# Performance work log

Hardware: AMD Instinct MI355X
Metric: run time of the kernel (lower is better)

Reference implementation:

```python
import jax, jax.numpy as jnp
import numpy as np

N_NODES = 100000
N_EDGES = 1600000
IN_DIM = 128
HID = 128
OUT_DIM = 64
N_LAYERS = 2
MAXK = 16


def setup_inputs() -> dict:
    key = jax.random.key(0)
    ks = jax.random.split(key, 8)
    x = jax.random.normal(ks[0], (N_NODES, IN_DIM), dtype=jnp.float32)
    src = jax.random.randint(ks[1], (N_EDGES,), 0, N_NODES, dtype=jnp.int32)
    dst = jax.random.randint(ks[2], (N_EDGES,), 0, N_NODES, dtype=jnp.int32)
    # Linear weights stored as [in, out] (y = x @ W + b), xavier-like scale
    s_in = float(np.sqrt(2.0 / (IN_DIM + HID)))
    s_h = float(np.sqrt(2.0 / (HID + HID)))
    s_out = float(np.sqrt(2.0 / (HID + OUT_DIM)))
    W_in = jax.random.normal(ks[3], (IN_DIM, HID), dtype=jnp.float32) * s_in
    b_in = jnp.zeros((HID,), dtype=jnp.float32)
    W_lin = jax.random.normal(ks[4], (N_LAYERS, HID, HID), dtype=jnp.float32) * s_h
    b_lin = jnp.zeros((N_LAYERS, HID), dtype=jnp.float32)
    eps = jnp.zeros((N_LAYERS,), dtype=jnp.float32)  # learn_eps=True, init_eps=0
    W_out = jax.random.normal(ks[5], (HID, OUT_DIM), dtype=jnp.float32) * s_out
    b_out = jnp.zeros((OUT_DIM,), dtype=jnp.float32)
    return {"x": x, "src": src, "dst": dst, "W_in": W_in, "b_in": b_in,
            "W_lin": W_lin, "b_lin": b_lin, "eps": eps,
            "W_out": W_out, "b_out": b_out}


def _maxk(x, k):
    # OPTMaxK: keep top-k entries per row (dim=1), zero the rest.
    _, idx = jax.lax.top_k(x, k)                      # [N, k]
    rows = jnp.arange(x.shape[0])[:, None]            # [N, 1]
    mask = jnp.zeros_like(x).at[rows, idx].set(1.0)
    return x * mask


def reference(x, src, dst, W_in, b_in, W_lin, b_lin, eps, W_out, b_out):
    n = x.shape[0]
    h = jax.nn.relu(x @ W_in + b_in)                  # lin_in + relu
    for i in range(N_LAYERS):
        h = h @ W_lin[i] + b_lin[i]                   # per-layer Linear
        h_sparse = _maxk(h, MAXK)                     # MaxK nonlinearity (dropout p=0 -> identity)
        # GIN sum aggregation over edges: neigh[v] = sum_{(u->v)} h_sparse[u]
        msg = jnp.take(h_sparse, src, axis=0)         # [E, HID] irregular gather
        neigh = jax.ops.segment_sum(msg, dst, num_segments=n)
        h = (1.0 + eps[i]) * h_sparse + neigh         # eps residual (apply_func=None, no norm)
    return h @ W_out + b_out
```

## Files before the change

kernel.cpp:

```cpp
#include <hip/hip_runtime.h>
#include <cstdint>
#include <cstddef>


typedef __attribute__((ext_vector_type(8))) short bf16x8;
typedef __attribute__((ext_vector_type(4))) float f32x4;

#define BSHIFT 8
#define NBUK 512

__device__ __forceinline__ unsigned rne_bf16(float v) {
  unsigned u = __float_as_uint(v);
  return (u + 0x7fffu + ((u >> 16) & 1u)) >> 16;
}

__global__ __launch_bounds__(256) void wt_build_all_kernel(
    const float* __restrict__ W_in, const float* __restrict__ W_lin,
    const float* __restrict__ W_out, short* __restrict__ out) {
  const int i = blockIdx.x * 256 + threadIdx.x;
  if (i >= 57344) return;
  const float* W;
  int nout, local;
  short* H;
  if (i < 16384) {
    W = W_in; nout = 128; local = i; H = out;
  } else if (i < 32768) {
    W = W_lin; nout = 128; local = i - 16384; H = out + 32768;
  } else if (i < 49152) {
    W = W_lin + 16384; nout = 128; local = i - 32768; H = out + 65536;
  } else {
    W = W_out; nout = 64; local = i - 49152; H = out + 98304;
  }
  const int nn = local >> 7, k = local & 127;
  const float v = W[k * nout + nn];
  const unsigned hb = rne_bf16(v);
  const float hf = __uint_as_float(hb << 16);
  const unsigned lb = rne_bf16(v - hf);
  H[local] = (short)hb;
  H[local + nout * 128] = (short)lb;
}

__global__ __launch_bounds__(256, 2) void gemm_in_kernel(
    const float* __restrict__ X, const short* __restrict__ WtH,
    const short* __restrict__ WtL, const float* __restrict__ bias,
    short* __restrict__ Yh, short* __restrict__ Yl, int nrows, int ntiles) {
  constexpr int NOUT = 128;
  constexpr int NT = NOUT / 16;
  constexpr int LDB = 128 * 2 + 16;
  constexpr int PLANE = NOUT * LDB;
  __shared__ char lds[2 * PLANE];

  const int tid = threadIdx.x;
  for (int u = tid; u < 2 * NOUT * 16; u += 256) {
    const int plane = u / (NOUT * 16);
    const int v = u % (NOUT * 16);
    const int nrow = v >> 4, seg = v & 15;
    const short* src = plane ? WtL : WtH;
    const float4 d = *(const float4*)&src[nrow * 128 + seg * 8];
    *(float4*)&lds[plane * PLANE + nrow * LDB + seg * 16] = d;
  }
  __syncthreads();

  const int lane = tid & 63;
  const int wv = tid >> 6;
  const int li = lane & 15;
  const int kg = lane >> 4;

  float bv[NT];
#pragma unroll
  for (int t = 0; t < NT; ++t) bv[t] = bias[t * 16 + li];

  for (int tile = blockIdx.x; tile < ntiles; tile += gridDim.x) {
    const int rowbase = tile * 256 + wv * 64;

    f32x4 acc[4][NT];
#pragma unroll
    for (int rg = 0; rg < 4; ++rg)
#pragma unroll
      for (int t = 0; t < NT; ++t) acc[rg][t] = (f32x4){0.f, 0.f, 0.f, 0.f};

#pragma unroll
    for (int c = 0; c < 4; ++c) {
      bf16x8 ah[4], al[4];
#pragma unroll
      for (int rg = 0; rg < 4; ++rg) {
        const int row = rowbase + rg * 16 + li;
        const int rowc = (row < nrows) ? row : (nrows - 1);
        const float* xrow = X + (size_t)rowc * 128 + c * 32 + kg * 8;
        const float4 p0 = *(const float4*)&xrow[0];
        const float4 p1 = *(const float4*)&xrow[4];
        const float f[8] = {p0.x, p0.y, p0.z, p0.w, p1.x, p1.y, p1.z, p1.w};
#pragma unroll
        for (int e = 0; e < 8; ++e) {
          const unsigned hb = rne_bf16(f[e]);
          const float hf = __uint_as_float(hb << 16);
          ah[rg][e] = (short)hb;
          al[rg][e] = (short)rne_bf16(f[e] - hf);
        }
      }
      const int kb = c * 64 + kg * 16;
#pragma unroll
      for (int t = 0; t < NT; ++t) {
        const int boff = (t * 16 + li) * LDB + kb;
        const bf16x8 bh = *(const bf16x8*)&lds[boff];
        const bf16x8 bl = *(const bf16x8*)&lds[PLANE + boff];
#pragma unroll
        for (int rg = 0; rg < 4; ++rg) {
          acc[rg][t] =
              __builtin_amdgcn_mfma_f32_16x16x32_bf16(al[rg], bh, acc[rg][t], 0, 0, 0);
          acc[rg][t] =
              __builtin_amdgcn_mfma_f32_16x16x32_bf16(ah[rg], bl, acc[rg][t], 0, 0, 0);
          acc[rg][t] =
              __builtin_amdgcn_mfma_f32_16x16x32_bf16(ah[rg], bh, acc[rg][t], 0, 0, 0);
        }
      }
    }

#pragma unroll
    for (int rg = 0; rg < 4; ++rg) {
      const int orow = rowbase + rg * 16 + kg * 4;
#pragma unroll
      for (int t = 0; t < NT; ++t) {
        const int col = t * 16 + li;
#pragma unroll
        for (int r = 0; r < 4; ++r) {
          const int rr = orow + r;
          if (rr < nrows) {
            const float o = fmaxf(acc[rg][t][r] + bv[t], 0.f);
            const unsigned hb = rne_bf16(o);
            const float hf = __uint_as_float(hb << 16);
            Yh[(size_t)rr * 128 + col] = (short)hb;
            Yl[(size_t)rr * 128 + col] = (short)rne_bf16(o - hf);
          }
        }
      }
    }
  }
}

template <int NOUT>
__global__ __launch_bounds__(256, 2) void gemm_pl_kernel(
    const short* __restrict__ Xh, const short* __restrict__ Xl,
    const short* __restrict__ WtH, const short* __restrict__ WtL,
    const float* __restrict__ bias, float* __restrict__ Y, int nrows,
    int ntiles) {
  constexpr int NT = NOUT / 16;
  constexpr int LDB = 128 * 2 + 16;
  constexpr int PLANE = NOUT * LDB;
  __shared__ char lds[2 * PLANE];

  const int tid = threadIdx.x;
  for (int u = tid; u < 2 * NOUT * 16; u += 256) {
    const int plane = u / (NOUT * 16);
    const int v = u % (NOUT * 16);
    const int nrow = v >> 4, seg = v & 15;
    const short* src = plane ? WtL : WtH;
    const float4 d = *(const float4*)&src[nrow * 128 + seg * 8];
    *(float4*)&lds[plane * PLANE + nrow * LDB + seg * 16] = d;
  }
  __syncthreads();

  const int lane = tid & 63;
  const int wv = tid >> 6;
  const int li = lane & 15;
  const int kg = lane >> 4;

  float bv[NT];
#pragma unroll
  for (int t = 0; t < NT; ++t) bv[t] = bias[t * 16 + li];

  for (int tile = blockIdx.x; tile < ntiles; tile += gridDim.x) {
    const int rowbase = tile * 256 + wv * 64;

    f32x4 acc[4][NT];
#pragma unroll
    for (int rg = 0; rg < 4; ++rg)
#pragma unroll
      for (int t = 0; t < NT; ++t) acc[rg][t] = (f32x4){0.f, 0.f, 0.f, 0.f};

#pragma unroll
    for (int c = 0; c < 4; ++c) {
      bf16x8 ah[4], al[4];
#pragma unroll
      for (int rg = 0; rg < 4; ++rg) {
        const int row = rowbase + rg * 16 + li;
        const int rowc = (row < nrows) ? row : (nrows - 1);
        ah[rg] = *(const bf16x8*)&Xh[(size_t)rowc * 128 + c * 32 + kg * 8];
        al[rg] = *(const bf16x8*)&Xl[(size_t)rowc * 128 + c * 32 + kg * 8];
      }
      const int kb = c * 64 + kg * 16;
#pragma unroll
      for (int t = 0; t < NT; ++t) {
        const int boff = (t * 16 + li) * LDB + kb;
        const bf16x8 bh = *(const bf16x8*)&lds[boff];
        const bf16x8 bl = *(const bf16x8*)&lds[PLANE + boff];
#pragma unroll
        for (int rg = 0; rg < 4; ++rg) {
          acc[rg][t] =
              __builtin_amdgcn_mfma_f32_16x16x32_bf16(al[rg], bh, acc[rg][t], 0, 0, 0);
          acc[rg][t] =
              __builtin_amdgcn_mfma_f32_16x16x32_bf16(ah[rg], bl, acc[rg][t], 0, 0, 0);
          acc[rg][t] =
              __builtin_amdgcn_mfma_f32_16x16x32_bf16(ah[rg], bh, acc[rg][t], 0, 0, 0);
        }
      }
    }

#pragma unroll
    for (int rg = 0; rg < 4; ++rg) {
      const int orow = rowbase + rg * 16 + kg * 4;
#pragma unroll
      for (int t = 0; t < NT; ++t) {
        const int col = t * 16 + li;
#pragma unroll
        for (int r = 0; r < 4; ++r) {
          const int rr = orow + r;
          if (rr < nrows) Y[(size_t)rr * NOUT + col] = acc[rg][t][r] + bv[t];
        }
      }
    }
  }
}

__global__ __launch_bounds__(256) void maxk_kernel(
    const float* __restrict__ T, unsigned char* __restrict__ Cs,
    float* __restrict__ Vs, int nrows) {
  const int lane = threadIdx.x & 63;
  const int wid = threadIdx.x >> 6;
  const int sub = lane >> 4;
  const int s = lane & 15;
  const int shift = sub * 16;
  const unsigned below = (1u << s) - 1u;
  const int nquads = (nrows + 3) / 4;

  for (int quad = blockIdx.x * 4 + wid; quad < nquads; quad += gridDim.x * 4) {
    const int row = quad * 4 + sub;
    const int rowc = (row < nrows) ? row : (nrows - 1);
    const float* Trow = T + (size_t)rowc * 128;

    float v[8];
    unsigned k[8];
#pragma unroll
    for (int j = 0; j < 8; ++j) {
      v[j] = Trow[j * 16 + s];
      const unsigned u = __float_as_uint(v[j]);
      k[j] = u ^ (((unsigned)((int)u >> 31)) | 0x80000000u);
    }

    unsigned P = 0;
    int kth = 16;
    int sz = 128;
    bool done = false;
    for (int b = 31; b >= 0; --b) {
      const unsigned tgt = (P >> b) | 1u;
      int c = 0;
#pragma unroll
      for (int j = 0; j < 8; ++j) {
        const unsigned long long bal = __ballot((k[j] >> b) == tgt);
        c += __popc((unsigned)((bal >> shift) & 0xFFFFull));
      }
      if (!done) {
        if (c >= kth) {
          P |= (1u << b);
          sz = c;
        } else {
          sz -= c;
          kth -= c;
        }
        done = (sz == kth);
      }
      if (__all(done)) break;
    }
    if (done) P -= 1u;

    unsigned gtm[8], eqm[8];
    int gt_total = 0;
#pragma unroll
    for (int j = 0; j < 8; ++j) {
      const unsigned long long gb = __ballot(k[j] > P);
      const unsigned long long eb = __ballot(k[j] == P);
      gtm[j] = (unsigned)((gb >> shift) & 0xFFFFull);
      eqm[j] = (unsigned)((eb >> shift) & 0xFFFFull);
      gt_total += __popc(gtm[j]);
    }
    const int need = 16 - gt_total;
    int gt_pre = 0, eq_pre = 0;
#pragma unroll
    for (int j = 0; j < 8; ++j) {
      const bool isgt = k[j] > P;
      const bool iseq = k[j] == P;
      const int gtb = gt_pre + __popc(gtm[j] & below);
      const int eqb = eq_pre + __popc(eqm[j] & below);
      if (row < nrows && (isgt || (iseq && eqb < need))) {
        const int rank = gtb + (isgt ? min(eqb, need) : eqb);
        Vs[(size_t)row * 16 + rank] = v[j];
        Cs[(size_t)row * 16 + rank] = (unsigned char)(j * 16 + s);
      }
      gt_pre += __popc(gtm[j]);
      eq_pre += __popc(eqm[j]);
    }
  }
}

__global__ __launch_bounds__(256) void bhist_kernel(const int* __restrict__ dst,
                                                    int* __restrict__ BC,
                                                    int E) {
  __shared__ int bh[NBUK];
  for (int i = threadIdx.x; i < NBUK; i += 256) bh[i] = 0;
  __syncthreads();
  const int stride = gridDim.x * 256;
  for (int e = blockIdx.x * 256 + threadIdx.x; e < E; e += stride)
    atomicAdd(&bh[dst[e] >> BSHIFT], 1);
  __syncthreads();
  for (int i = threadIdx.x; i < NBUK; i += 256)
    if (bh[i]) atomicAdd(&BC[i], bh[i]);
}

__global__ __launch_bounds__(NBUK) void bscan_kernel(
    const int* __restrict__ BC, int* __restrict__ bases,
    int* __restrict__ bcur, int* __restrict__ rs, int n, int E) {
  __shared__ int sc[NBUK];
  const int t = threadIdx.x;
  const int c = BC[t];
  sc[t] = c;
  __syncthreads();
  for (int st = 1; st < NBUK; st <<= 1) {
    const int v = sc[t];
    const int u = (t >= st) ? sc[t - st] : 0;
    __syncthreads();
    sc[t] = v + u;
    __syncthreads();
  }
  const int excl = sc[t] - c;
  bases[t] = excl;
  bcur[t] = excl;
  if (t == 0) rs[n] = E;
}

__global__ __launch_bounds__(256) void bin_kernel(
    const int* __restrict__ src, const int* __restrict__ dst,
    int* __restrict__ bcur, uint2* __restrict__ binned, int E, int chunk) {
  __shared__ int cnt[NBUK], off[NBUK], gbase[NBUK];
  __shared__ unsigned short bktof[4096];
  __shared__ uint2 buf[4096];
  const int t = threadIdx.x;
  const int beg = blockIdx.x * chunk;
  const int m = min(chunk, E - beg);
  if (m <= 0) return;

  for (int i = t; i < NBUK; i += 256) cnt[i] = 0;
  __syncthreads();

  int d[16], s[16], lp[16], bk[16];
#pragma unroll
  for (int i = 0; i < 16; ++i) {
    const int j = i * 256 + t;
    if (j < m) {
      d[i] = dst[beg + j];
      s[i] = src[beg + j];
      bk[i] = d[i] >> BSHIFT;
      lp[i] = atomicAdd(&cnt[bk[i]], 1);
    } else {
      bk[i] = -1;
    }
  }
  __syncthreads();

  for (int i = t; i < NBUK; i += 256) off[i] = cnt[i];
  __syncthreads();
  for (int st = 1; st < NBUK; st <<= 1) {
    int v0, v1, u0, u1;
    {
      const int i0 = t, i1 = t + 256;
      v0 = off[i0]; u0 = (i0 >= st) ? off[i0 - st] : 0;
      v1 = off[i1]; u1 = (i1 >= st) ? off[i1 - st] : 0;
    }
    __syncthreads();
    off[t] = v0 + u0;
    off[t + 256] = v1 + u1;
    __syncthreads();
  }

  for (int i = t; i < NBUK; i += 256) {
    const int c = cnt[i];
    if (c > 0) {
      gbase[i] = atomicAdd(&bcur[i], c);
      const int e0 = off[i] - c;
      for (int k = 0; k < c; ++k) bktof[e0 + k] = (unsigned short)i;
    }
  }
  __syncthreads();

#pragma unroll
  for (int i = 0; i < 16; ++i) {
    if (bk[i] >= 0) {
      buf[(off[bk[i]] - cnt[bk[i]]) + lp[i]] =
          make_uint2((unsigned)d[i], (unsigned)s[i]);
    }
  }
  __syncthreads();

  for (int j = t; j < m; j += 256) {
    const int b = bktof[j];
    const int e0 = off[b] - cnt[b];
    binned[gbase[b] + (j - e0)] = buf[j];
  }
}

__global__ __launch_bounds__(256) void bbuild_kernel(
    const int* __restrict__ bases, const int* __restrict__ BC,
    const uint2* __restrict__ binned, int* __restrict__ rs,
    int* __restrict__ csr_src, int n) {
  __shared__ int nd[256], sc[256], cur[256];
  const int b = blockIdx.x;
  const int t = threadIdx.x;
  const int base = bases[b];
  const int count = BC[b];
  const int node0 = b << BSHIFT;

  nd[t] = 0;
  __syncthreads();
  for (int i = t; i < count; i += 256)
    atomicAdd(&nd[binned[base + i].x & 255], 1);
  __syncthreads();

  sc[t] = nd[t];
  __syncthreads();
  for (int st = 1; st < 256; st <<= 1) {
    const int v = sc[t];
    const int u = (t >= st) ? sc[t - st] : 0;
    __syncthreads();
    sc[t] = v + u;
    __syncthreads();
  }
  const int excl = sc[t] - nd[t];
  cur[t] = excl;
  if (node0 + t < n) rs[node0 + t] = base + excl;
  __syncthreads();

  for (int i = t; i < count; i += 256) {
    const uint2 p = binned[base + i];
    const int pos = atomicAdd(&cur[p.x & 255], 1);
    csr_src[base + pos] = (int)p.y;
  }
}

__global__ __launch_bounds__(256) void gather6_kernel(
    const int* __restrict__ rs, const int* __restrict__ csr_src,
    const unsigned char* __restrict__ Cs, const float* __restrict__ Vs,
    const float* __restrict__ eps_p, short* __restrict__ Ah,
    short* __restrict__ Al, int nrows) {
  __shared__ __align__(16) float sv[4][16][16];
  __shared__ __align__(16) unsigned char scb[4][16][16];
  __shared__ float accb[4][4 * 132];
  const int lane = threadIdx.x & 63;
  const int wid = threadIdx.x >> 6;
  const float e1 = 1.0f + *eps_p;
  const int ee = lane >> 2;
  const int q = lane & 3;
  const int g = lane >> 4;
  const int p = lane & 15;
  float* acc = accb[wid];
  float4* acc4 = (float4*)acc;

  for (int r = blockIdx.x * 4 + wid; r < nrows; r += gridDim.x * 4) {
    for (int i = lane; i < 132; i += 64)
      acc4[i] = make_float4(0.f, 0.f, 0.f, 0.f);

    const int beg = rs[r], end = rs[r + 1];
    for (int base = beg; base < end; base += 16) {
      const int cnt = min(16, end - base);
      if (ee < cnt) {
        const int s = csr_src[base + ee];
        if (q == 0) {
          const int4 c4 = *(const int4*)&Cs[(size_t)s * 16];
          *(int4*)&scb[wid][ee][0] = c4;
        }
        const float4 v = *(const float4*)&Vs[(size_t)s * 16 + q * 4];
        *(float4*)&sv[wid][ee][q * 4] = v;
      }
      for (int e = 0; e < cnt; e += 4) {
        const int eg = e + g;
        if (eg < cnt) {
          const int col = scb[wid][eg][p];
          const float val = sv[wid][eg][p];
          acc[g * 132 + col] += val;
        }
      }
    }
    if (lane < 16) {
      const int c = Cs[(size_t)r * 16 + lane];
      const float v = Vs[(size_t)r * 16 + lane];
      acc[c] += e1 * v;
    }
    const float a0 = acc[lane] + acc[132 + lane] + acc[264 + lane] +
                     acc[396 + lane];
    const float a1 = acc[64 + lane] + acc[132 + 64 + lane] +
                     acc[264 + 64 + lane] + acc[396 + 64 + lane];
    const unsigned h0 = rne_bf16(a0);
    const unsigned h1 = rne_bf16(a1);
    Ah[(size_t)r * 128 + lane] = (short)h0;
    Ah[(size_t)r * 128 + 64 + lane] = (short)h1;
    Al[(size_t)r * 128 + lane] =
        (short)rne_bf16(a0 - __uint_as_float(h0 << 16));
    Al[(size_t)r * 128 + 64 + lane] =
        (short)rne_bf16(a1 - __uint_as_float(h1 << 16));
  }
}

extern "C" void kernel_launch(void* const* d_in, const int* in_sizes, int n_in,
                              void* d_out, int out_size, void* d_ws,
                              size_t ws_size, hipStream_t stream) {
  const float* x = (const float*)d_in[0];
  const int* src = (const int*)d_in[1];
  const int* dst = (const int*)d_in[2];
  const float* W_in = (const float*)d_in[3];
  const float* b_in = (const float*)d_in[4];
  const float* W_lin = (const float*)d_in[5];
  const float* b_lin = (const float*)d_in[6];
  const float* eps = (const float*)d_in[7];
  const float* W_out = (const float*)d_in[8];
  const float* b_out = (const float*)d_in[9];
  float* out = (float*)d_out;

  const int n = in_sizes[0] / 128;
  const int E = in_sizes[1];

  char* w = (char*)d_ws;
  float* B = (float*)w;               w += (size_t)n * 128 * 4;
  unsigned char* Cs = (unsigned char*)w; w += (size_t)n * 16;
  float* Vs = (float*)w;              w += (size_t)n * 16 * 4;
  int* rs = (int*)w;                  w += (size_t)(n + 1) * 4;
  int* csr_src = (int*)w;             w += (size_t)E * 4;
  uint2* binned = (uint2*)w;          w += (size_t)E * 8;
  int* BC = (int*)w;                  w += NBUK * 4;
  int* bases = (int*)w;               w += NBUK * 4;
  int* bcur = (int*)w;                w += NBUK * 4;
  short* wtAll = (short*)w;           w += (size_t)114688 * 2;
  short* Ah = (short*)w;              w += (size_t)n * 128 * 2;
  short* Al = (short*)w;              w += (size_t)n * 128 * 2;

  short* wtIn = wtAll;
  short* wtL0 = wtAll + 32768;
  short* wtL1 = wtAll + 65536;
  short* wtOut = wtAll + 98304;

  const int ptiles = (n + 255) / 256;
  const int nbuk_eff = (n + 255) >> BSHIFT;
  const int chunk = 4000;
  const int cblocks = (E + chunk - 1) / chunk;
  const dim3 blk(256);

  hipMemsetAsync(BC, 0, NBUK * 4, stream);
  bhist_kernel<<<256, blk, 0, stream>>>(dst, BC, E);
  bscan_kernel<<<1, NBUK, 0, stream>>>(BC, bases, bcur, rs, n, E);
  bin_kernel<<<cblocks, blk, 0, stream>>>(src, dst, bcur, binned, E, chunk);
  bbuild_kernel<<<nbuk_eff, blk, 0, stream>>>(bases, BC, binned, rs, csr_src,
                                              n);

  wt_build_all_kernel<<<(57344 + 255) / 256, blk, 0, stream>>>(W_in, W_lin,
                                                               W_out, wtAll);

  gemm_in_kernel<<<ptiles, blk, 0, stream>>>(x, wtIn, wtIn + 16384, b_in, Ah,
                                             Al, n, ptiles);

  for (int l = 0; l < 2; ++l) {
    short* wt = l ? wtL1 : wtL0;
    gemm_pl_kernel<128><<<ptiles, blk, 0, stream>>>(
        Ah, Al, wt, wt + 16384, b_lin + (size_t)l * 128, B, n, ptiles);
    maxk_kernel<<<2048, blk, 0, stream>>>(B, Cs, Vs, n);
    gather6_kernel<<<2048, blk, 0, stream>>>(rs, csr_src, Cs, Vs, eps + l, Ah,
                                             Al, n);
  }

  gemm_pl_kernel<64><<<ptiles, blk, 0, stream>>>(Ah, Al, wtOut, wtOut + 8192,
                                                 b_out, out, n, ptiles);
}
```

Baseline: 393.8 us.

## Fuse per-layer GEMM with top-k selection in registers

Replaces the separate layer GEMM plus maxk kernels with one kernel that runs the top-16 radix selection directly on the MFMA accumulator fragments. The accumulator layout puts each row's 128 columns across 16 lanes by 8 tiles, which matches the selection's wave-ballot scheme. This drops the fp32 intermediate buffer write and reread (about 51 MB per layer) and one launch per layer. The cost is more register pressure and serial selection work inside the GEMM kernel, which may lower occupancy or overlap.

```diff
diff --git a/kernel.cpp b/kernel.cpp
--- a/kernel.cpp
+++ b/kernel.cpp
@@ -12,6 +12,70 @@
 __device__ __forceinline__ unsigned rne_bf16(float v) {
   unsigned u = __float_as_uint(v);
   return (u + 0x7fffu + ((u >> 16) & 1u)) >> 16;
+}
+
+__device__ __forceinline__ void row_select16(
+    const float v[8], int row, int nrows, int shift, int s, unsigned below,
+    unsigned char* __restrict__ Cs, float* __restrict__ Vs) {
+  unsigned k[8];
+#pragma unroll
+  for (int j = 0; j < 8; ++j) {
+    const unsigned u = __float_as_uint(v[j]);
+    k[j] = u ^ (((unsigned)((int)u >> 31)) | 0x80000000u);
+  }
+
+  unsigned P = 0;
+  int kth = 16;
+  int sz = 128;
+  bool done = false;
+  for (int b = 31; b >= 0; --b) {
+    const unsigned tgt = (P >> b) | 1u;
+    int c = 0;
+#pragma unroll
+    for (int j = 0; j < 8; ++j) {
+      const unsigned long long bal = __ballot((k[j] >> b) == tgt);
+      c += __popc((unsigned)((bal >> shift) & 0xFFFFull));
+    }
+    if (!done) {
+      if (c >= kth) {
+        P |= (1u << b);
+        sz = c;
+      } else {
+        sz -= c;
+        kth -= c;
+      }
+      done = (sz == kth);
+    }
+    if (__all(done)) break;
+  }
+  if (done) P -= 1u;
+
+  unsigned gtm[8], eqm[8];
+  int gt_total = 0;
+#pragma unroll
+  for (int j = 0; j < 8; ++j) {
+    const unsigned long long gb = __ballot(k[j] > P);
+    const unsigned long long eb = __ballot(k[j] == P);
+    gtm[j] = (unsigned)((gb >> shift) & 0xFFFFull);
+    eqm[j] = (unsigned)((eb >> shift) & 0xFFFFull);
+    gt_total += __popc(gtm[j]);
+  }
+  const int need = 16 - gt_total;
+  int gt_pre = 0, eq_pre = 0;
+#pragma unroll
+  for (int j = 0; j < 8; ++j) {
+    const bool isgt = k[j] > P;
+    const bool iseq = k[j] == P;
+    const int gtb = gt_pre + __popc(gtm[j] & below);
+    const int eqb = eq_pre + __popc(eqm[j] & below);
+    if (row < nrows && (isgt || (iseq && eqb < need))) {
+      const int rank = gtb + (isgt ? min(eqb, need) : eqb);
+      Vs[(size_t)row * 16 + rank] = v[j];
+      Cs[(size_t)row * 16 + rank] = (unsigned char)(j * 16 + s);
+    }
+    gt_pre += __popc(gtm[j]);
+    eq_pre += __popc(eqm[j]);
+  }
 }
 
 __global__ __launch_bounds__(256) void wt_build_all_kernel(
@@ -138,6 +202,90 @@
   }
 }
 
+__global__ __launch_bounds__(256, 2) void gemm_maxk_kernel(
+    const short* __restrict__ Xh, const short* __restrict__ Xl,
+    const short* __restrict__ WtH, const short* __restrict__ WtL,
+    const float* __restrict__ bias, unsigned char* __restrict__ Cs,
+    float* __restrict__ Vs, int nrows, int ntiles) {
+  constexpr int NOUT = 128;
+  constexpr int NT = NOUT / 16;
+  constexpr int LDB = 128 * 2 + 16;
+  constexpr int PLANE = NOUT * LDB;
+  __shared__ char lds[2 * PLANE];
+
+  const int tid = threadIdx.x;
+  for (int u = tid; u < 2 * NOUT * 16; u += 256) {
+    const int plane = u / (NOUT * 16);
+    const int v = u % (NOUT * 16);
+    const int nrow = v >> 4, seg = v & 15;
+    const short* src = plane ? WtL : WtH;
+    const float4 d = *(const float4*)&src[nrow * 128 + seg * 8];
+    *(float4*)&lds[plane * PLANE + nrow * LDB + seg * 16] = d;
+  }
+  __syncthreads();
+
+  const int lane = tid & 63;
+  const int wv = tid >> 6;
+  const int li = lane & 15;
+  const int kg = lane >> 4;
+  const int shift = kg * 16;
+  const unsigned below = (1u << li) - 1u;
+
+  float bv[NT];
+#pragma unroll
+  for (int t = 0; t < NT; ++t) bv[t] = bias[t * 16 + li];
+
+  for (int tile = blockIdx.x; tile < ntiles; tile += gridDim.x) {
+    const int rowbase = tile * 256 + wv * 64;
+
+    f32x4 acc[4][NT];
+#pragma unroll
+    for (int rg = 0; rg < 4; ++rg)
+#pragma unroll
+      for (int t = 0; t < NT; ++t) acc[rg][t] = (f32x4){0.f, 0.f, 0.f, 0.f};
+
+#pragma unroll
+    for (int c = 0; c < 4; ++c) {
+      bf16x8 ah[4], al[4];
+#pragma unroll
+      for (int rg = 0; rg < 4; ++rg) {
+        const int row = rowbase + rg * 16 + li;
+        const int rowc = (row < nrows) ? row : (nrows - 1);
+        ah[rg] = *(const bf16x8*)&Xh[(size_t)rowc * 128 + c * 32 + kg * 8];
+        al[rg] = *(const bf16x8*)&Xl[(size_t)rowc * 128 + c * 32 + kg * 8];
+      }
+      const int kb = c * 64 + kg * 16;
+#pragma unroll
+      for (int t = 0; t < NT; ++t) {
+        const int boff = (t * 16 + li) * LDB + kb;
+        const bf16x8 bh = *(const bf16x8*)&lds[boff];
+        const bf16x8 bl = *(const bf16x8*)&lds[PLANE + boff];
+#pragma unroll
+        for (int rg = 0; rg < 4; ++rg) {
+          acc[rg][t] =
+              __builtin_amdgcn_mfma_f32_16x16x32_bf16(al[rg], bh, acc[rg][t], 0, 0, 0);
+          acc[rg][t] =
+              __builtin_amdgcn_mfma_f32_16x16x32_bf16(ah[rg], bl, acc[rg][t], 0, 0, 0);
+          acc[rg][t] =
+              __builtin_amdgcn_mfma_f32_16x16x32_bf16(ah[rg], bh, acc[rg][t], 0, 0, 0);
+        }
+      }
+    }
+
+#pragma unroll
+    for (int rg = 0; rg < 4; ++rg) {
+#pragma unroll
+      for (int r = 0; r < 4; ++r) {
+        const int row = rowbase + rg * 16 + kg * 4 + r;
+        float v[8];
+#pragma unroll
+        for (int t = 0; t < NT; ++t) v[t] = acc[rg][t][r] + bv[t];
+        row_select16(v, row, nrows, shift, li, below, Cs, Vs);
+      }
+    }
+  }
+}
+
 template <int NOUT>
 __global__ __launch_bounds__(256, 2) void gemm_pl_kernel(
     const short* __restrict__ Xh, const short* __restrict__ Xl,
@@ -218,86 +366,6 @@
           if (rr < nrows) Y[(size_t)rr * NOUT + col] = acc[rg][t][r] + bv[t];
         }
       }
-    }
-  }
-}
-
-__global__ __launch_bounds__(256) void maxk_kernel(
-    const float* __restrict__ T, unsigned char* __restrict__ Cs,
-    float* __restrict__ Vs, int nrows) {
-  const int lane = threadIdx.x & 63;
-  const int wid = threadIdx.x >> 6;
-  const int sub = lane >> 4;
-  const int s = lane & 15;
-  const int shift = sub * 16;
-  const unsigned below = (1u << s) - 1u;
-  const int nquads = (nrows + 3) / 4;
-
-  for (int quad = blockIdx.x * 4 + wid; quad < nquads; quad += gridDim.x * 4) {
-    const int row = quad * 4 + sub;
-    const int rowc = (row < nrows) ? row : (nrows - 1);
-    const float* Trow = T + (size_t)rowc * 128;
-
-    float v[8];
-    unsigned k[8];
-#pragma unroll
-    for (int j = 0; j < 8; ++j) {
-      v[j] = Trow[j * 16 + s];
-      const unsigned u = __float_as_uint(v[j]);
-      k[j] = u ^ (((unsigned)((int)u >> 31)) | 0x80000000u);
-    }
-
-    unsigned P = 0;
-    int kth = 16;
-    int sz = 128;
-    bool done = false;
-    for (int b = 31; b >= 0; --b) {
-      const unsigned tgt = (P >> b) | 1u;
-      int c = 0;
-#pragma unroll
-      for (int j = 0; j < 8; ++j) {
-        const unsigned long long bal = __ballot((k[j] >> b) == tgt);
-        c += __popc((unsigned)((bal >> shift) & 0xFFFFull));
-      }
-      if (!done) {
-        if (c >= kth) {
-          P |= (1u << b);
-          sz = c;
-        } else {
-          sz -= c;
-          kth -= c;
-        }
-        done = (sz == kth);
-      }
-      if (__all(done)) break;
-    }
-    if (done) P -= 1u;
-
-    unsigned gtm[8], eqm[8];
-    int gt_total = 0;
-#pragma unroll
-    for (int j = 0; j < 8; ++j) {
-      const unsigned long long gb = __ballot(k[j] > P);
-      const unsigned long long eb = __ballot(k[j] == P);
-      gtm[j] = (unsigned)((gb >> shift) & 0xFFFFull);
-      eqm[j] = (unsigned)((eb >> shift) & 0xFFFFull);
-      gt_total += __popc(gtm[j]);
-    }
-    const int need = 16 - gt_total;
-    int gt_pre = 0, eq_pre = 0;
-#pragma unroll
-    for (int j = 0; j < 8; ++j) {
-      const bool isgt = k[j] > P;
-      const bool iseq = k[j] == P;
-      const int gtb = gt_pre + __popc(gtm[j] & below);
-      const int eqb = eq_pre + __popc(eqm[j] & below);
-      if (row < nrows && (isgt || (iseq && eqb < need))) {
-        const int rank = gtb + (isgt ? min(eqb, need) : eqb);
-        Vs[(size_t)row * 16 + rank] = v[j];
-        Cs[(size_t)row * 16 + rank] = (unsigned char)(j * 16 + s);
-      }
-      gt_pre += __popc(gtm[j]);
-      eq_pre += __popc(eqm[j]);
     }
   }
 }
@@ -527,7 +595,6 @@
   const int E = in_sizes[1];
 
   char* w = (char*)d_ws;
-  float* B = (float*)w;               w += (size_t)n * 128 * 4;
   unsigned char* Cs = (unsigned char*)w; w += (size_t)n * 16;
   float* Vs = (float*)w;              w += (size_t)n * 16 * 4;
   int* rs = (int*)w;                  w += (size_t)(n + 1) * 4;
@@ -566,9 +633,8 @@
 
   for (int l = 0; l < 2; ++l) {
     short* wt = l ? wtL1 : wtL0;
-    gemm_pl_kernel<128><<<ptiles, blk, 0, stream>>>(
-        Ah, Al, wt, wt + 16384, b_lin + (size_t)l * 128, B, n, ptiles);
-    maxk_kernel<<<2048, blk, 0, stream>>>(B, Cs, Vs, n);
+    gemm_maxk_kernel<<<ptiles, blk, 0, stream>>>(
+        Ah, Al, wt, wt + 16384, b_lin + (size_t)l * 128, Cs, Vs, n, ptiles);
     gather6_kernel<<<2048, blk, 0, stream>>>(rs, csr_src, Cs, Vs, eps + l, Ah,
                                              Al, n);
   }
```

Result: slower. 441.9 us (+12.2%).
